# Kernel optimization log

Hardware: AMD Instinct MI355X
Metric: run time of the kernel (lower is better)

The kernel has to match this reference:

```python
import jax, jax.numpy as jnp
import numpy as np

H = 256  # hidden_channels
N_USERS = 100000
N_MOVIES = 50000
N_EDGES = 500000


def setup_inputs() -> dict:
    key = jax.random.key(0)
    k1, k2, k3, k4, k5, k6, k7 = jax.random.split(key, 7)
    user_emb = jax.random.normal(k1, (N_USERS, H), dtype=jnp.float32)
    movie_emb = jax.random.normal(k2, (N_MOVIES, H), dtype=jnp.float32)
    edge_label_index = jax.random.randint(k3, (2, N_EDGES), 0, N_MOVIES, dtype=jnp.int64)
    # Linear(2H, H) and Linear(H, 1) params, torch default init scale
    s1 = 1.0 / np.sqrt(2 * H)
    s2 = 1.0 / np.sqrt(H)
    W1 = jax.random.uniform(k4, (2 * H, H), dtype=jnp.float32, minval=-s1, maxval=s1)
    b1 = jax.random.uniform(k5, (H,), dtype=jnp.float32, minval=-s1, maxval=s1)
    W2 = jax.random.uniform(k6, (H, 1), dtype=jnp.float32, minval=-s2, maxval=s2)
    b2 = jax.random.uniform(k7, (1,), dtype=jnp.float32, minval=-s2, maxval=s2)
    return {"user_emb": user_emb, "movie_emb": movie_emb,
            "edge_label_index": edge_label_index,
            "W1": W1, "b1": b1, "W2": W2, "b2": b2}


def reference(user_emb, movie_emb, edge_label_index, W1, b1, W2, b2):
    u = user_emb[edge_label_index[0]]    # [E, H]
    m = movie_emb[edge_label_index[1]]   # [E, H]
    x = jnp.concatenate([u, m], axis=-1)  # [E, 2H]
    x = jax.nn.relu(x @ W1 + b1)          # [E, H]
    return x @ W2 + b2                    # [E, 1]
```

## Files before the change

kernel.cpp:

```cpp
#include <hip/hip_runtime.h>
#include <hip/hip_bf16.h>

typedef __attribute__((ext_vector_type(8))) short v8s;
typedef __attribute__((ext_vector_type(4))) float v4f;

constexpr int H  = 256;
constexpr int K2 = 512;
constexpr int XS = 72;
constexpr int WS = 72;

__device__ inline unsigned short f2bf(float f) {
    unsigned int u = __builtin_bit_cast(unsigned int, f);
    u += 0x7FFFu + ((u >> 16) & 1u);
    return (unsigned short)(u >> 16);
}
__device__ inline float bf2f(unsigned short s) {
    return __builtin_bit_cast(float, (unsigned int)s << 16);
}

__global__ void w1_transpose_kernel(const float* __restrict__ w1,
                                    unsigned short* __restrict__ w1t) {
    __shared__ float tile[32][33];
    const int bk = blockIdx.x;
    const int bn = blockIdx.y;
    const int tx = threadIdx.x & 31;
    const int ty8 = threadIdx.x >> 5;
#pragma unroll
    for (int i = 0; i < 4; ++i) {
        int ty = i * 8 + ty8;
        tile[ty][tx] = w1[(size_t)(bk * 32 + ty) * H + bn * 32 + tx];
    }
    __syncthreads();
#pragma unroll
    for (int i = 0; i < 4; ++i) {
        int ty = i * 8 + ty8;
        w1t[(size_t)(bn * 32 + ty) * K2 + bk * 32 + tx] = f2bf(tile[tx][ty]);
    }
}

__global__ __launch_bounds__(512, 4) void emb_gemm_fused_kernel(
    const float* __restrict__ user_emb,
    const float* __restrict__ movie_emb,
    const unsigned short* __restrict__ w1t,
    const float* __restrict__ b1,
    unsigned short* __restrict__ P,
    unsigned short* __restrict__ Q,
    const int n_users, const int n_movies, const int nbu)
{
    __shared__ unsigned short Xs[64 * XS];
    __shared__ unsigned short Wts[H * WS];

    const int  isMovie = (blockIdx.x >= nbu) ? 1 : 0;
    const float* emb  = isMovie ? movie_emb : user_emb;
    unsigned short* outp = isMovie ? Q : P;
    const int  M     = isMovie ? n_movies : n_users;
    const int  kofs  = isMovie ? 256 : 0;
    const long m0    = (long)(blockIdx.x - (isMovie ? nbu : 0)) * 64;

    const int t    = threadIdx.x;
    const int wave = t >> 6;
    const int lane = t & 63;
    const int wm   = wave >> 2;
    const int wn   = wave & 3;
    const int quad = lane >> 4;
    const int l16  = lane & 15;

    const int xr = t >> 3;
    const int xc = t & 7;
    long mr = m0 + xr; if (mr >= M) mr = M - 1;
    const float* arow = emb + (size_t)mr * H;

    const int wr  = t >> 3;
    const int wc8 = t & 7;
    const unsigned short* wbase = w1t + (size_t)wr * K2 + kofs + wc8 * 8;

    v4f acc[2][4];
#pragma unroll
    for (int mt = 0; mt < 2; ++mt)
#pragma unroll
        for (int nt = 0; nt < 4; ++nt)
            acc[mt][nt] = (v4f){0.f, 0.f, 0.f, 0.f};

    v4f a0 = *(const v4f*)(arow + xc * 8);
    v4f a1 = *(const v4f*)(arow + xc * 8 + 4);
    v8s wq[4];
#pragma unroll
    for (int j = 0; j < 4; ++j)
        wq[j] = *(const v8s*)(wbase + (size_t)j * 64 * K2);

    for (int kt = 0; kt < 4; ++kt) {
        __syncthreads();
        {
            v8s xv;
#pragma unroll
            for (int i = 0; i < 4; ++i) { xv[i] = (short)f2bf(a0[i]); xv[4+i] = (short)f2bf(a1[i]); }
            *(v8s*)(Xs + xr * XS + xc * 8) = xv;
        }
#pragma unroll
        for (int j = 0; j < 4; ++j)
            *(v8s*)(Wts + (j * 64 + wr) * WS + wc8 * 8) = wq[j];
        if (kt < 3) {
            const int kn = kt + 1;
            a0 = *(const v4f*)(arow + kn * 64 + xc * 8);
            a1 = *(const v4f*)(arow + kn * 64 + xc * 8 + 4);
#pragma unroll
            for (int j = 0; j < 4; ++j)
                wq[j] = *(const v8s*)(wbase + (size_t)j * 64 * K2 + kn * 64);
        }
        __syncthreads();
#pragma unroll
        for (int ks = 0; ks < 2; ++ks) {
            v8s af[2], bf[4];
#pragma unroll
            for (int mt = 0; mt < 2; ++mt)
                af[mt] = *(const v8s*)(Xs + (wm * 32 + mt * 16 + l16) * XS + ks * 32 + quad * 8);
#pragma unroll
            for (int nt = 0; nt < 4; ++nt)
                bf[nt] = *(const v8s*)(Wts + (wn * 64 + nt * 16 + l16) * WS + ks * 32 + quad * 8);
#pragma unroll
            for (int mt = 0; mt < 2; ++mt)
#pragma unroll
                for (int nt = 0; nt < 4; ++nt)
                    acc[mt][nt] = __builtin_amdgcn_mfma_f32_16x16x32_bf16(
                        af[mt], bf[nt], acc[mt][nt], 0, 0, 0);
        }
    }

    float bv[4];
#pragma unroll
    for (int nt = 0; nt < 4; ++nt)
        bv[nt] = isMovie ? 0.f : b1[wn * 64 + nt * 16 + l16];

#pragma unroll
    for (int mt = 0; mt < 2; ++mt) {
#pragma unroll
        for (int j = 0; j < 4; ++j) {
            long m = m0 + wm * 32 + mt * 16 + quad * 4 + j;
            if (m < M) {
#pragma unroll
                for (int nt = 0; nt < 4; ++nt) {
                    int n = wn * 64 + nt * 16 + l16;
                    outp[(size_t)m * H + n] = f2bf(acc[mt][nt][j] + bv[nt]);
                }
            }
        }
    }
}

__global__ __launch_bounds__(256, 8) void edge_score_kernel(
    const unsigned short* __restrict__ P,
    const unsigned short* __restrict__ Q,
    const int* __restrict__ eli,
    const float* __restrict__ w2,
    const float* __restrict__ b2,
    float* __restrict__ out,
    const int E, const int n_users, const int n_movies)
{
    const int t   = threadIdx.x;
    const int hw  = t >> 5;
    const int l32 = t & 31;

    float w2v[8];
    {
        v4f a = *(const v4f*)(w2 + l32 * 8);
        v4f b = *(const v4f*)(w2 + l32 * 8 + 4);
#pragma unroll
        for (int i = 0; i < 4; ++i) { w2v[i] = a[i]; w2v[4 + i] = b[i]; }
    }
    const float b2v = b2[0];
    const long base = (long)blockIdx.x * 64;

    int us[8], ms[8];
#pragma unroll
    for (int i = 0; i < 8; ++i) {
        long e = base + i * 8 + hw;
        long ec = (e < E) ? e : 0;
        int u = eli[ec];
        int m = eli[(long)E + ec];
        us[i] = u < 0 ? 0 : (u >= n_users  ? n_users  - 1 : u);
        ms[i] = m < 0 ? 0 : (m >= n_movies ? n_movies - 1 : m);
    }

    v8s pv = *(const v8s*)(P + (size_t)us[0] * H + l32 * 8);
    v8s qv = *(const v8s*)(Q + (size_t)ms[0] * H + l32 * 8);

#pragma unroll
    for (int i = 0; i < 8; ++i) {
        v8s pn, qn;
        if (i < 7) {
            pn = *(const v8s*)(P + (size_t)us[i + 1] * H + l32 * 8);
            qn = *(const v8s*)(Q + (size_t)ms[i + 1] * H + l32 * 8);
        }
        float s = 0.f;
#pragma unroll
        for (int j = 0; j < 8; ++j) {
            float h = bf2f((unsigned short)pv[j]) + bf2f((unsigned short)qv[j]);
            h = h > 0.f ? h : 0.f;
            s += h * w2v[j];
        }
        s += __shfl_xor(s, 1, 64);
        s += __shfl_xor(s, 2, 64);
        s += __shfl_xor(s, 4, 64);
        s += __shfl_xor(s, 8, 64);
        s += __shfl_xor(s, 16, 64);
        long e = base + i * 8 + hw;
        if (l32 == 0 && e < E) out[e] = s + b2v;
        pv = pn; qv = qn;
    }
}

constexpr int BMF = 64;
__global__ __launch_bounds__(512, 4) void edge_decoder_kernel(
    const float* __restrict__ user_emb, const float* __restrict__ movie_emb,
    const int* __restrict__ eli, const unsigned short* __restrict__ w1t,
    const float* __restrict__ b1, const float* __restrict__ w2,
    const float* __restrict__ b2, float* __restrict__ out,
    const int E, const int n_users, const int n_movies)
{
    __shared__ unsigned short Xs[BMF * XS];
    __shared__ unsigned short Wts[H * WS];
    __shared__ float red[4][BMF];
    const int t = threadIdx.x, wave = t >> 6, lane = t & 63;
    const int wm = wave >> 2, wn = wave & 3, quad = lane >> 4, l16 = lane & 15;
    const long e0 = (long)blockIdx.x * BMF;
    const int xr = t >> 3, xc = t & 7;
    long eg = e0 + xr; if (eg >= E) eg = 0;
    int iu = eli[eg], im = eli[(long)E + eg];
    iu = iu < 0 ? 0 : (iu >= n_users ? n_users - 1 : iu);
    im = im < 0 ? 0 : (im >= n_movies ? n_movies - 1 : im);
    const float* urow = user_emb + (size_t)iu * H;
    const float* mrow = movie_emb + (size_t)im * H;
    const int wr = t >> 3, wc8 = t & 7;
    const unsigned short* wbase = w1t + (size_t)wr * K2 + wc8 * 8;
    v4f acc[2][4];
#pragma unroll
    for (int mt = 0; mt < 2; ++mt)
#pragma unroll
        for (int nt = 0; nt < 4; ++nt) acc[mt][nt] = (v4f){0.f,0.f,0.f,0.f};
    v4f xq0 = *(const v4f*)(urow + xc * 8);
    v4f xq1 = *(const v4f*)(urow + xc * 8 + 4);
    v8s wq[4];
#pragma unroll
    for (int j = 0; j < 4; ++j) wq[j] = *(const v8s*)(wbase + (size_t)j * 64 * K2);
    for (int kt = 0; kt < 8; ++kt) {
        __syncthreads();
        { v8s xv;
#pragma unroll
          for (int i = 0; i < 4; ++i) xv[i] = (short)f2bf(xq0[i]);
#pragma unroll
          for (int i = 0; i < 4; ++i) xv[4+i] = (short)f2bf(xq1[i]);
          *(v8s*)(Xs + xr * XS + xc * 8) = xv; }
#pragma unroll
        for (int j = 0; j < 4; ++j) *(v8s*)(Wts + (j * 64 + wr) * WS + wc8 * 8) = wq[j];
        if (kt < 7) {
            const int kn = kt + 1, koff = (kn * 64) & 255;
            const float* src = ((kn < 4) ? urow : mrow) + koff + xc * 8;
            xq0 = *(const v4f*)(src); xq1 = *(const v4f*)(src + 4);
#pragma unroll
            for (int j = 0; j < 4; ++j) wq[j] = *(const v8s*)(wbase + (size_t)j * 64 * K2 + kn * 64);
        }
        __syncthreads();
#pragma unroll
        for (int ks = 0; ks < 2; ++ks) {
            v8s af[2], bf[4];
#pragma unroll
            for (int mt = 0; mt < 2; ++mt)
                af[mt] = *(const v8s*)(Xs + (wm * 32 + mt * 16 + l16) * XS + ks * 32 + quad * 8);
#pragma unroll
            for (int nt = 0; nt < 4; ++nt)
                bf[nt] = *(const v8s*)(Wts + (wn * 64 + nt * 16 + l16) * WS + ks * 32 + quad * 8);
#pragma unroll
            for (int mt = 0; mt < 2; ++mt)
#pragma unroll
                for (int nt = 0; nt < 4; ++nt)
                    acc[mt][nt] = __builtin_amdgcn_mfma_f32_16x16x32_bf16(af[mt], bf[nt], acc[mt][nt], 0, 0, 0);
        }
    }
    float b1v[4], w2v[4];
#pragma unroll
    for (int nt = 0; nt < 4; ++nt) {
        int n = wn * 64 + nt * 16 + l16;
        b1v[nt] = b1[n]; w2v[nt] = w2[n];
    }
    const float b2v = b2[0];
#pragma unroll
    for (int mt = 0; mt < 2; ++mt) {
        float s[4] = {0.f,0.f,0.f,0.f};
#pragma unroll
        for (int nt = 0; nt < 4; ++nt)
#pragma unroll
            for (int j = 0; j < 4; ++j) {
                float h = acc[mt][nt][j] + b1v[nt];
                h = h > 0.f ? h : 0.f;
                s[j] += h * w2v[nt];
            }
#pragma unroll
        for (int j = 0; j < 4; ++j) {
            float v = s[j];
            v += __shfl_xor(v, 1, 64); v += __shfl_xor(v, 2, 64);
            v += __shfl_xor(v, 4, 64); v += __shfl_xor(v, 8, 64);
            if (l16 == 0) red[wn][wm * 32 + mt * 16 + quad * 4 + j] = v;
        }
    }
    __syncthreads();
    if (t < BMF) {
        long e = e0 + t;
        if (e < E) out[e] = red[0][t] + red[1][t] + red[2][t] + red[3][t] + b2v;
    }
}

extern "C" void kernel_launch(void* const* d_in, const int* in_sizes, int n_in,
                              void* d_out, int out_size, void* d_ws, size_t ws_size,
                              hipStream_t stream) {
    const float* user_emb  = (const float*)d_in[0];
    const float* movie_emb = (const float*)d_in[1];
    const int*   eli       = (const int*)d_in[2];
    const float* w1        = (const float*)d_in[3];
    const float* b1        = (const float*)d_in[4];
    const float* w2        = (const float*)d_in[5];
    const float* b2        = (const float*)d_in[6];
    float*       out       = (float*)d_out;

    const int E        = out_size;
    const int n_users  = in_sizes[0] / H;
    const int n_movies = in_sizes[1] / H;

    unsigned short* w1t = (unsigned short*)d_ws;
    const size_t w1t_bytes = (size_t)K2 * H * 2;
    const size_t p_bytes   = (size_t)n_users  * H * 2;
    const size_t q_bytes   = (size_t)n_movies * H * 2;

    w1_transpose_kernel<<<dim3(16, 8), 256, 0, stream>>>(w1, w1t);

    if (ws_size >= w1t_bytes + p_bytes + q_bytes) {
        unsigned short* P = (unsigned short*)((char*)d_ws + w1t_bytes);
        unsigned short* Q = (unsigned short*)((char*)d_ws + w1t_bytes + p_bytes);
        const int nbu = (n_users  + 63) / 64;
        const int nbm = (n_movies + 63) / 64;
        emb_gemm_fused_kernel<<<nbu + nbm, 512, 0, stream>>>(
            user_emb, movie_emb, w1t, b1, P, Q, n_users, n_movies, nbu);
        edge_score_kernel<<<(E + 63) / 64, 256, 0, stream>>>(
            P, Q, eli, w2, b2, out, E, n_users, n_movies);
    } else {
        edge_decoder_kernel<<<(E + BMF - 1) / BMF, 512, 0, stream>>>(
            user_emb, movie_emb, eli, w1t, b1, w2, b2, out, E, n_users, n_movies);
    }
}
```

Measured before the change: 286.5 us.

## Stage full X tile once and read W1 fragments directly from global

Rewrites the node-embedding GEMM to use 256-thread blocks. Each block converts the whole 64x256 embedding tile to bf16 in shared memory with a single barrier. The W1 shared-memory staging and per-k-step barriers are removed: each wave now loads its B fragments straight from the global/L2-resident transposed weights, and each wave computes all 64 rows (4x4 MFMA tiles). This removes repeated synchronisation and LDS traffic for W, at the cost of more global loads of W per block and a larger accumulator register footprint.

```diff
diff --git a/kernel.cpp b/kernel.cpp
--- a/kernel.cpp
+++ b/kernel.cpp
@@ -4,10 +4,11 @@
 typedef __attribute__((ext_vector_type(8))) short v8s;
 typedef __attribute__((ext_vector_type(4))) float v4f;
 
-constexpr int H  = 256;
-constexpr int K2 = 512;
-constexpr int XS = 72;
-constexpr int WS = 72;
+constexpr int H   = 256;
+constexpr int K2  = 512;
+constexpr int XS  = 72;
+constexpr int WS  = 72;
+constexpr int XS2 = 264;
 
 __device__ inline unsigned short f2bf(float f) {
     unsigned int u = __builtin_bit_cast(unsigned int, f);
@@ -38,7 +39,7 @@
     }
 }
 
-__global__ __launch_bounds__(512, 4) void emb_gemm_fused_kernel(
+__global__ __launch_bounds__(256, 4) void emb_gemm2_kernel(
     const float* __restrict__ user_emb,
     const float* __restrict__ movie_emb,
     const unsigned short* __restrict__ w1t,
@@ -47,78 +48,68 @@
     unsigned short* __restrict__ Q,
     const int n_users, const int n_movies, const int nbu)
 {
-    __shared__ unsigned short Xs[64 * XS];
-    __shared__ unsigned short Wts[H * WS];
-
-    const int  isMovie = (blockIdx.x >= nbu) ? 1 : 0;
+    __shared__ unsigned short Xs[64 * XS2];
+
+    const int isMovie = (blockIdx.x >= nbu) ? 1 : 0;
     const float* emb  = isMovie ? movie_emb : user_emb;
     unsigned short* outp = isMovie ? Q : P;
-    const int  M     = isMovie ? n_movies : n_users;
-    const int  kofs  = isMovie ? 256 : 0;
-    const long m0    = (long)(blockIdx.x - (isMovie ? nbu : 0)) * 64;
+    const int  M    = isMovie ? n_movies : n_users;
+    const int  kofs = isMovie ? 256 : 0;
+    const long m0   = (long)(blockIdx.x - (isMovie ? nbu : 0)) * 64;
 
     const int t    = threadIdx.x;
-    const int wave = t >> 6;
+    const int wn   = t >> 6;
     const int lane = t & 63;
-    const int wm   = wave >> 2;
-    const int wn   = wave & 3;
     const int quad = lane >> 4;
     const int l16  = lane & 15;
 
-    const int xr = t >> 3;
-    const int xc = t & 7;
-    long mr = m0 + xr; if (mr >= M) mr = M - 1;
-    const float* arow = emb + (size_t)mr * H;
-
-    const int wr  = t >> 3;
-    const int wc8 = t & 7;
-    const unsigned short* wbase = w1t + (size_t)wr * K2 + kofs + wc8 * 8;
-
-    v4f acc[2][4];
-#pragma unroll
-    for (int mt = 0; mt < 2; ++mt)
+    {
+        const int xr = t >> 2;
+        const int xc = t & 3;
+        long mr = m0 + xr; if (mr >= M) mr = M - 1;
+        const float* arow = emb + (size_t)mr * H + xc * 64;
+        unsigned short* dst = Xs + xr * XS2 + xc * 64;
+#pragma unroll
+        for (int it = 0; it < 4; ++it) {
+            v4f a0 = *(const v4f*)(arow + it * 16);
+            v4f a1 = *(const v4f*)(arow + it * 16 + 4);
+            v4f a2 = *(const v4f*)(arow + it * 16 + 8);
+            v4f a3 = *(const v4f*)(arow + it * 16 + 12);
+            v8s x0, x1;
+#pragma unroll
+            for (int i = 0; i < 4; ++i) { x0[i] = (short)f2bf(a0[i]); x0[4+i] = (short)f2bf(a1[i]); }
+#pragma unroll
+            for (int i = 0; i < 4; ++i) { x1[i] = (short)f2bf(a2[i]); x1[4+i] = (short)f2bf(a3[i]); }
+            *(v8s*)(dst + it * 16)     = x0;
+            *(v8s*)(dst + it * 16 + 8) = x1;
+        }
+    }
+
+    v4f acc[4][4];
+#pragma unroll
+    for (int mt = 0; mt < 4; ++mt)
 #pragma unroll
         for (int nt = 0; nt < 4; ++nt)
             acc[mt][nt] = (v4f){0.f, 0.f, 0.f, 0.f};
 
-    v4f a0 = *(const v4f*)(arow + xc * 8);
-    v4f a1 = *(const v4f*)(arow + xc * 8 + 4);
-    v8s wq[4];
-#pragma unroll
-    for (int j = 0; j < 4; ++j)
-        wq[j] = *(const v8s*)(wbase + (size_t)j * 64 * K2);
-
+    __syncthreads();
+
+    const unsigned short* wbase = w1t + (size_t)(wn * 64 + l16) * K2 + kofs + quad * 8;
+
+#pragma unroll
     for (int kt = 0; kt < 4; ++kt) {
-        __syncthreads();
-        {
-            v8s xv;
-#pragma unroll
-            for (int i = 0; i < 4; ++i) { xv[i] = (short)f2bf(a0[i]); xv[4+i] = (short)f2bf(a1[i]); }
-            *(v8s*)(Xs + xr * XS + xc * 8) = xv;
-        }
-#pragma unroll
-        for (int j = 0; j < 4; ++j)
-            *(v8s*)(Wts + (j * 64 + wr) * WS + wc8 * 8) = wq[j];
-        if (kt < 3) {
-            const int kn = kt + 1;
-            a0 = *(const v4f*)(arow + kn * 64 + xc * 8);
-            a1 = *(const v4f*)(arow + kn * 64 + xc * 8 + 4);
-#pragma unroll
-            for (int j = 0; j < 4; ++j)
-                wq[j] = *(const v8s*)(wbase + (size_t)j * 64 * K2 + kn * 64);
-        }
-        __syncthreads();
 #pragma unroll
         for (int ks = 0; ks < 2; ++ks) {
-            v8s af[2], bf[4];
-#pragma unroll
-            for (int mt = 0; mt < 2; ++mt)
-                af[mt] = *(const v8s*)(Xs + (wm * 32 + mt * 16 + l16) * XS + ks * 32 + quad * 8);
+            const int k0 = kt * 64 + ks * 32;
+            v8s af[4], bf[4];
 #pragma unroll
             for (int nt = 0; nt < 4; ++nt)
-                bf[nt] = *(const v8s*)(Wts + (wn * 64 + nt * 16 + l16) * WS + ks * 32 + quad * 8);
-#pragma unroll
-            for (int mt = 0; mt < 2; ++mt)
+                bf[nt] = *(const v8s*)(wbase + (size_t)nt * 16 * K2 + k0);
+#pragma unroll
+            for (int mt = 0; mt < 4; ++mt)
+                af[mt] = *(const v8s*)(Xs + (mt * 16 + l16) * XS2 + k0 + quad * 8);
+#pragma unroll
+            for (int mt = 0; mt < 4; ++mt)
 #pragma unroll
                 for (int nt = 0; nt < 4; ++nt)
                     acc[mt][nt] = __builtin_amdgcn_mfma_f32_16x16x32_bf16(
@@ -132,10 +123,10 @@
         bv[nt] = isMovie ? 0.f : b1[wn * 64 + nt * 16 + l16];
 
 #pragma unroll
-    for (int mt = 0; mt < 2; ++mt) {
+    for (int mt = 0; mt < 4; ++mt) {
 #pragma unroll
         for (int j = 0; j < 4; ++j) {
-            long m = m0 + wm * 32 + mt * 16 + quad * 4 + j;
+            long m = m0 + mt * 16 + quad * 4 + j;
             if (m < M) {
 #pragma unroll
                 for (int nt = 0; nt < 4; ++nt) {
@@ -337,7 +328,7 @@
         unsigned short* Q = (unsigned short*)((char*)d_ws + w1t_bytes + p_bytes);
         const int nbu = (n_users  + 63) / 64;
         const int nbm = (n_movies + 63) / 64;
-        emb_gemm_fused_kernel<<<nbu + nbm, 512, 0, stream>>>(
+        emb_gemm2_kernel<<<nbu + nbm, 256, 0, stream>>>(
             user_emb, movie_emb, w1t, b1, P, Q, n_users, n_movies, nbu);
         edge_score_kernel<<<(E + 63) / 64, 256, 0, stream>>>(
             P, Q, eli, w2, b2, out, E, n_users, n_movies);
```

Result: slower. 310.2 us (+8.3%).
